# Performance work log

Measured on AMD Instinct MI355X. Metric: run time of the kernel, lower is better.

The kernel has to match this reference:

```python
import jax, jax.numpy as jnp
import numpy as np

POOL_SIZES = (1, 3, 6, 8)
EPS = 1e-5


def conv1x1(x, W, b):
    # x: [b, cin, h, w], W: [cout, cin], b: [cout]
    return jnp.einsum('bchw,oc->bohw', x, W) + b[None, :, None, None]


def ppm(x):
    # x: [b, c, h, w] -> [b, c, S] with S = sum(p*p); H,W divisible by each p
    b, c, h, w = x.shape
    outs = []
    for p in POOL_SIZES:
        pooled = x.reshape(b, c, p, h // p, p, w // p).mean(axis=(3, 5))
        outs.append(pooled.reshape(b, c, p * p))
    return jnp.concatenate(outs, axis=-1)


def setup_inputs() -> dict:
    key = jax.random.key(0)
    ks = jax.random.split(key, 8)
    B, Cin, H, W = 4, 512, 120, 120
    Ck, Cv, Cout = 256, 256, 512
    x = jax.random.normal(ks[0], (B, Cin, H, W), dtype=jnp.float32)
    sc = lambda cin: 1.0 / np.sqrt(cin)
    Wk = jax.random.normal(ks[1], (Ck, Cin), dtype=jnp.float32) * sc(Cin)
    bk = jnp.zeros((Ck,), jnp.float32)
    gamma = jnp.ones((Ck,), jnp.float32)
    beta = jnp.zeros((Ck,), jnp.float32)
    mean = jax.random.normal(ks[2], (Ck,), dtype=jnp.float32) * 0.1
    var = jax.random.uniform(ks[3], (Ck,), dtype=jnp.float32, minval=0.5, maxval=1.5)
    Wv = jax.random.normal(ks[4], (Cv, Cin), dtype=jnp.float32) * sc(Cin)
    bv = jnp.zeros((Cv,), jnp.float32)
    # original inits Conv_Out to zero; use random weights for a nontrivial baseline
    Wo = jax.random.normal(ks[5], (Cout, Cv), dtype=jnp.float32) * sc(Cv)
    bo = jnp.zeros((Cout,), jnp.float32)
    return {'x': x, 'Wk': Wk, 'bk': bk, 'gamma': gamma, 'beta': beta,
            'mean': mean, 'var': var, 'Wv': Wv, 'bv': bv, 'Wo': Wo, 'bo': bo}


def reference(x, Wk, bk, gamma, beta, mean, var, Wv, bv, Wo, bo):
    b, _, h, w = x.shape
    ck = Wk.shape[0]
    cv = Wv.shape[0]
    # shared Conv_Key / Conv_Query: conv1x1 -> BN (inference) -> ReLU
    kq = conv1x1(x, Wk, bk)
    inv = gamma / jnp.sqrt(var + EPS)
    kq = jax.nn.relu(kq * inv[None, :, None, None] + (beta - mean * inv)[None, :, None, None])
    value = ppm(conv1x1(x, Wv, bv)).transpose(0, 2, 1)      # [b, S, cv]
    key = ppm(kq)                                            # [b, ck, S]
    query = kq.reshape(b, ck, h * w).transpose(0, 2, 1)      # [b, hw, ck]
    scores = jnp.einsum('bnc,bcs->bns', query, key) * (ck ** -0.5)
    attn = jax.nn.softmax(scores, axis=-1)                   # [b, hw, S]
    agg = jnp.einsum('bns,bsv->bnv', attn, value)            # [b, hw, cv]
    agg = agg.transpose(0, 2, 1).reshape(b, cv, h, w)
    return conv1x1(agg, Wo, bo)
```

## Files before the change

kernel.cpp:

```cpp
#include <hip/hip_runtime.h>
#include <cstdint>
#include <cstddef>

#define HW 14400
#define WIDTH 120
#define S_TOT 110

typedef unsigned short u16;
typedef __attribute__((ext_vector_type(8))) short bf16x8;
typedef __attribute__((ext_vector_type(4))) float f32x4;

__device__ __forceinline__ u16 f2bf(float x) {
  unsigned u = __float_as_uint(x);
  unsigned r = (u + 0x7fffu + ((u >> 16) & 1u)) >> 16;
  return (u16)r;
}
__device__ __forceinline__ float bf2f(u16 h) {
  return __uint_as_float((unsigned)h << 16);
}

__device__ __forceinline__ void async16(void* lds, const void* g) {
  __builtin_amdgcn_global_load_lds(
      (const __attribute__((address_space(1))) void*)g,
      (__attribute__((address_space(3))) void*)lds, 16, 0, 0);
}

__global__ __launch_bounds__(256) void pool_kernel(const float* __restrict__ in,
                                                   float* __restrict__ outp) {
  __shared__ float part[576];
  const float* plane = in + (size_t)blockIdx.x * HW;
  int t = threadIdx.x;
  for (int bb = t; bb < 576; bb += 256) {
    int by = bb / 24, bx = bb % 24;
    const float* p0 = plane + (by * 5) * WIDTH + bx * 5;
    float s = 0.f;
#pragma unroll
    for (int yy = 0; yy < 5; ++yy)
#pragma unroll
      for (int xx = 0; xx < 5; ++xx) s += p0[yy * WIDTH + xx];
    part[bb] = s;
  }
  __syncthreads();
  if (t < S_TOT) {
    float s = 0.f;
    if (t == 0) {
      for (int i = 0; i < 576; ++i) s += part[i];
      s *= (1.f / 14400.f);
    } else if (t < 10) {
      int idx = t - 1, i = idx / 3, j = idx % 3;
      for (int a = 0; a < 8; ++a)
        for (int c = 0; c < 8; ++c) s += part[(i * 8 + a) * 24 + (j * 8 + c)];
      s *= (1.f / 1600.f);
    } else if (t < 46) {
      int idx = t - 10, i = idx / 6, j = idx % 6;
      for (int a = 0; a < 4; ++a)
        for (int c = 0; c < 4; ++c) s += part[(i * 4 + a) * 24 + (j * 4 + c)];
      s *= (1.f / 400.f);
    } else {
      int idx = t - 46, i = idx / 8, j = idx % 8;
      for (int a = 0; a < 3; ++a)
        for (int c = 0; c < 3; ++c) s += part[(i * 3 + a) * 24 + (j * 3 + c)];
      s *= (1.f / 225.f);
    }
    outp[(size_t)blockIdx.x * S_TOT + t] = s;
  }
}

__global__ __launch_bounds__(256) void convert_w(const float* __restrict__ in,
                                                 u16* __restrict__ hi,
                                                 u16* __restrict__ lo, int n) {
  int i = blockIdx.x * 256 + threadIdx.x;
  if (i < n) {
    float v = in[i];
    u16 h = f2bf(v);
    hi[i] = h;
    lo[i] = f2bf(v - bf2f(h));
  }
}

template <int CIN>
__global__ __launch_bounds__(256) void convert_t(const float* __restrict__ X,
                                                 u16* __restrict__ xth,
                                                 u16* __restrict__ xtl) {
  __shared__ float ls[64][65];
  int b = blockIdx.z;
  int n0 = blockIdx.x * 64, k0 = blockIdx.y * 64;
  int t = threadIdx.x;
  int rt = t >> 4, c4 = (t & 15) * 4;
#pragma unroll
  for (int rr = 0; rr < 4; ++rr) {
    int kk = rr * 16 + rt;
    float4 v = *(const float4*)&X[((size_t)(b * CIN + k0 + kk)) * HW + n0 + c4];
    ls[kk][c4] = v.x; ls[kk][c4 + 1] = v.y; ls[kk][c4 + 2] = v.z; ls[kk][c4 + 3] = v.w;
  }
  __syncthreads();
#pragma unroll
  for (int rr = 0; rr < 4; ++rr) {
    int nn = rr * 16 + rt;
    float v0 = ls[c4 + 0][nn], v1 = ls[c4 + 1][nn], v2 = ls[c4 + 2][nn], v3 = ls[c4 + 3][nn];
    ushort4 oh, ol;
    oh.x = f2bf(v0); ol.x = f2bf(v0 - bf2f(oh.x));
    oh.y = f2bf(v1); ol.y = f2bf(v1 - bf2f(oh.y));
    oh.z = f2bf(v2); ol.z = f2bf(v2 - bf2f(oh.z));
    oh.w = f2bf(v3); ol.w = f2bf(v3 - bf2f(oh.w));
    size_t idx = ((size_t)(b * HW + n0 + nn)) * CIN + k0 + c4;
    *(ushort4*)&xth[idx] = oh;
    *(ushort4*)&xtl[idx] = ol;
  }
}

template <int K, int M_TOT, bool BNRELU>
__global__ __launch_bounds__(256) void gemm_mfma(
    const u16* __restrict__ Ah, const u16* __restrict__ Al,
    const u16* __restrict__ Bh, const u16* __restrict__ Bl,
    float* __restrict__ C,
    const float* __restrict__ p0, const float* __restrict__ p1,
    const float* __restrict__ p2, const float* __restrict__ p3,
    const float* __restrict__ p4) {
  constexpr int NSTEP = K / 32;
  __shared__ alignas(16) u16 sAh[256 * 32];
  __shared__ alignas(16) u16 sAl[256 * 32];
  __shared__ alignas(16) u16 sBh[64 * 32];
  __shared__ alignas(16) u16 sBl[64 * 32];
  __shared__ float sP0[256], sP1[256];

  int t = threadIdx.x, w = t >> 6, l = t & 63;
  int b = blockIdx.z;
  int n0 = blockIdx.x * 64;
  int m0 = blockIdx.y * 256;

  if (BNRELU) {
    int m = m0 + t;
    float iv = p1[m] * rsqrtf(p4[m] + 1e-5f);
    sP0[t] = iv;
    sP1[t] = (p0[m] - p3[m]) * iv + p2[m];
  } else {
    sP0[t] = p0[m0 + t];
  }

  int crow = l >> 2;
  int cbyte = (l & 3) * 16;
  const size_t bOff = (size_t)b * HW;

  f32x4 acc[4][4];
#pragma unroll
  for (int i = 0; i < 4; ++i)
#pragma unroll
    for (int j = 0; j < 4; ++j) acc[i][j] = (f32x4){0.f, 0.f, 0.f, 0.f};

  int fr = l & 15, fk = (l >> 4) * 8;

  for (int ks = 0; ks < NSTEP; ++ks) {
    int k0 = ks * 32;
#pragma unroll
    for (int c = 0; c < 10; ++c) {
      int i = w * 10 + c;
      const u16* g;
      u16* d;
      if (i < 16) {
        g = Ah + (size_t)(m0 + i * 16 + crow) * K + k0;
        d = sAh + i * 512;
      } else if (i < 32) {
        g = Al + (size_t)(m0 + (i - 16) * 16 + crow) * K + k0;
        d = sAl + (i - 16) * 512;
      } else if (i < 36) {
        g = Bh + (bOff + n0 + (i - 32) * 16 + crow) * K + k0;
        d = sBh + (i - 32) * 512;
      } else {
        g = Bl + (bOff + n0 + (i - 36) * 16 + crow) * K + k0;
        d = sBl + (i - 36) * 512;
      }
      async16((char*)d, (const char*)g + cbyte);
    }
    __syncthreads();

    bf16x8 ah[4], al[4], bh[4], bl[4];
#pragma unroll
    for (int mt = 0; mt < 4; ++mt) {
      int r = w * 64 + mt * 16 + fr;
      ah[mt] = *(const bf16x8*)&sAh[r * 32 + fk];
      al[mt] = *(const bf16x8*)&sAl[r * 32 + fk];
    }
#pragma unroll
    for (int nt = 0; nt < 4; ++nt) {
      int r = nt * 16 + fr;
      bh[nt] = *(const bf16x8*)&sBh[r * 32 + fk];
      bl[nt] = *(const bf16x8*)&sBl[r * 32 + fk];
    }
#pragma unroll
    for (int mt = 0; mt < 4; ++mt)
#pragma unroll
      for (int nt = 0; nt < 4; ++nt) {
        acc[mt][nt] = __builtin_amdgcn_mfma_f32_16x16x32_bf16(ah[mt], bh[nt], acc[mt][nt], 0, 0, 0);
        acc[mt][nt] = __builtin_amdgcn_mfma_f32_16x16x32_bf16(ah[mt], bl[nt], acc[mt][nt], 0, 0, 0);
        acc[mt][nt] = __builtin_amdgcn_mfma_f32_16x16x32_bf16(al[mt], bh[nt], acc[mt][nt], 0, 0, 0);
      }
    __syncthreads();
  }

#pragma unroll
  for (int mt = 0; mt < 4; ++mt) {
    int lmBase = w * 64 + mt * 16 + (l >> 4) * 4;
#pragma unroll
    for (int nt = 0; nt < 4; ++nt) {
      int n = n0 + nt * 16 + fr;
#pragma unroll
      for (int r = 0; r < 4; ++r) {
        int lm = lmBase + r;
        float v = acc[mt][nt][r];
        if (BNRELU)
          v = fmaxf(v * sP0[lm] + sP1[lm], 0.f);
        else
          v = v + sP0[lm];
        C[((size_t)(b * M_TOT + m0 + lm)) * HW + n] = v;
      }
    }
  }
}

__global__ __launch_bounds__(256) void value_kernel(
    const float* __restrict__ Wv, const float* __restrict__ xp,
    const float* __restrict__ bv, u16* __restrict__ vth,
    u16* __restrict__ vtl) {
  int b = blockIdx.x >> 7, s = blockIdx.x & 127;
  int t = threadIdx.x;
  size_t o = ((size_t)(b * 256 + t)) * 128 + s;
  if (s >= S_TOT) { vth[o] = 0; vtl[o] = 0; return; }
  __shared__ float xs[512];
  for (int i = t; i < 512; i += 256) xs[i] = xp[((size_t)b * 512 + i) * S_TOT + s];
  __syncthreads();
  float accv = 0.f;
  const float* wv = Wv + (size_t)t * 512;
  for (int k = 0; k < 512; k += 4) {
    float4 w4 = *(const float4*)&wv[k];
    accv += w4.x * xs[k] + w4.y * xs[k + 1] + w4.z * xs[k + 2] + w4.w * xs[k + 3];
  }
  accv += bv[t];
  u16 h = f2bf(accv);
  vth[o] = h;
  vtl[o] = f2bf(accv - bf2f(h));
}

__global__ __launch_bounds__(256) void convert_key(const float* __restrict__ keyp,
                                                   u16* __restrict__ kth,
                                                   u16* __restrict__ ktl) {
  int b = blockIdx.x;
  int t = threadIdx.x;
  for (int i = t; i < 128 * 256; i += 256) {
    int s = i >> 8, c = i & 255;
    float v = (s < S_TOT) ? keyp[((size_t)(b * 256 + c)) * S_TOT + s] : 0.f;
    u16 h = f2bf(v);
    size_t o = ((size_t)(b * 128 + s)) * 256 + c;
    kth[o] = h;
    ktl[o] = f2bf(v - bf2f(h));
  }
}

__global__ __launch_bounds__(256) void attn_mfma(
    const u16* __restrict__ qh, const u16* __restrict__ ql,
    const u16* __restrict__ kh, const u16* __restrict__ kl,
    const u16* __restrict__ vh, const u16* __restrict__ vl,
    u16* __restrict__ aggh, u16* __restrict__ aggl) {
  __shared__ u16 Ph[64][136];
  __shared__ u16 Pl[64][136];
  int b = blockIdx.y, pix0 = blockIdx.x * 64;
  int t = threadIdx.x, w = t >> 6, l = t & 63;
  int fr = l & 15, q = l >> 4, fk = q * 8;

  f32x4 acc[7];
#pragma unroll
  for (int st = 0; st < 7; ++st) acc[st] = (f32x4){0.f, 0.f, 0.f, 0.f};

  const u16* qbh = qh + ((size_t)(b * HW + pix0 + w * 16 + fr)) * 256 + fk;
  const u16* qbl = ql + ((size_t)(b * HW + pix0 + w * 16 + fr)) * 256 + fk;
  const u16* kbh = kh + ((size_t)(b * 128 + fr)) * 256 + fk;
  const u16* kbl = kl + ((size_t)(b * 128 + fr)) * 256 + fk;

  for (int c0 = 0; c0 < 256; c0 += 32) {
    bf16x8 ah = *(const bf16x8*)(qbh + c0);
    bf16x8 al = *(const bf16x8*)(qbl + c0);
#pragma unroll
    for (int st = 0; st < 7; ++st) {
      bf16x8 bh = *(const bf16x8*)(kbh + (size_t)st * 16 * 256 + c0);
      bf16x8 bl = *(const bf16x8*)(kbl + (size_t)st * 16 * 256 + c0);
      acc[st] = __builtin_amdgcn_mfma_f32_16x16x32_bf16(ah, bh, acc[st], 0, 0, 0);
      acc[st] = __builtin_amdgcn_mfma_f32_16x16x32_bf16(ah, bl, acc[st], 0, 0, 0);
      acc[st] = __builtin_amdgcn_mfma_f32_16x16x32_bf16(al, bh, acc[st], 0, 0, 0);
    }
  }

#pragma unroll
  for (int st = 0; st < 7; ++st)
#pragma unroll
    for (int r = 0; r < 4; ++r) acc[st][r] *= 0.0625f;
  if (fr >= 14) {
#pragma unroll
    for (int r = 0; r < 4; ++r) acc[6][r] = -1e30f;
  }

#pragma unroll
  for (int r = 0; r < 4; ++r) {
    float m = -1e30f;
#pragma unroll
    for (int st = 0; st < 7; ++st) m = fmaxf(m, acc[st][r]);
    m = fmaxf(m, __shfl_xor(m, 1));
    m = fmaxf(m, __shfl_xor(m, 2));
    m = fmaxf(m, __shfl_xor(m, 4));
    m = fmaxf(m, __shfl_xor(m, 8));
    float s = 0.f;
#pragma unroll
    for (int st = 0; st < 7; ++st) {
      float e = __expf(acc[st][r] - m);
      acc[st][r] = e;
      s += e;
    }
    s += __shfl_xor(s, 1);
    s += __shfl_xor(s, 2);
    s += __shfl_xor(s, 4);
    s += __shfl_xor(s, 8);
    float inv = 1.f / s;
#pragma unroll
    for (int st = 0; st < 7; ++st) acc[st][r] *= inv;
  }

  int prow = w * 16 + q * 4;
#pragma unroll
  for (int st = 0; st < 7; ++st) {
    int s = st * 16 + fr;
#pragma unroll
    for (int r = 0; r < 4; ++r) {
      float v = acc[st][r];
      u16 h = f2bf(v);
      Ph[prow + r][s] = h;
      Pl[prow + r][s] = f2bf(v - bf2f(h));
    }
  }
  for (int i = t; i < 64 * 16; i += 256) {
    int rr = i >> 4, ss = 112 + (i & 15);
    Ph[rr][ss] = 0;
    Pl[rr][ss] = 0;
  }
  __syncthreads();

  f32x4 oacc[16];
#pragma unroll
  for (int nt = 0; nt < 16; ++nt) oacc[nt] = (f32x4){0.f, 0.f, 0.f, 0.f};

  const u16* vbh = vh + ((size_t)(b * 256 + fr)) * 128 + fk;
  const u16* vbl = vl + ((size_t)(b * 256 + fr)) * 128 + fk;

#pragma unroll
  for (int kc = 0; kc < 4; ++kc) {
    bf16x8 ah = *(const bf16x8*)&Ph[w * 16 + fr][kc * 32 + fk];
    bf16x8 al = *(const bf16x8*)&Pl[w * 16 + fr][kc * 32 + fk];
#pragma unroll
    for (int nt = 0; nt < 16; ++nt) {
      bf16x8 bh = *(const bf16x8*)(vbh + (size_t)nt * 16 * 128 + kc * 32);
      bf16x8 bl = *(const bf16x8*)(vbl + (size_t)nt * 16 * 128 + kc * 32);
      oacc[nt] = __builtin_amdgcn_mfma_f32_16x16x32_bf16(ah, bh, oacc[nt], 0, 0, 0);
      oacc[nt] = __builtin_amdgcn_mfma_f32_16x16x32_bf16(ah, bl, oacc[nt], 0, 0, 0);
      oacc[nt] = __builtin_amdgcn_mfma_f32_16x16x32_bf16(al, bh, oacc[nt], 0, 0, 0);
    }
  }

#pragma unroll
  for (int nt = 0; nt < 16; ++nt) {
    int cv = nt * 16 + fr;
#pragma unroll
    for (int r = 0; r < 4; ++r) {
      int pix = pix0 + w * 16 + q * 4 + r;
      float v = oacc[nt][r];
      u16 h = f2bf(v);
      size_t o = ((size_t)(b * HW + pix)) * 256 + cv;
      aggh[o] = h;
      aggl[o] = f2bf(v - bf2f(h));
    }
  }
}

extern "C" void kernel_launch(void* const* d_in, const int* in_sizes, int n_in,
                              void* d_out, int out_size, void* d_ws, size_t ws_size,
                              hipStream_t stream) {
  (void)in_sizes; (void)n_in; (void)out_size; (void)ws_size;
  const float* x     = (const float*)d_in[0];
  const float* Wk    = (const float*)d_in[1];
  const float* bk    = (const float*)d_in[2];
  const float* gamma = (const float*)d_in[3];
  const float* beta  = (const float*)d_in[4];
  const float* mean  = (const float*)d_in[5];
  const float* var   = (const float*)d_in[6];
  const float* Wv    = (const float*)d_in[7];
  const float* bv    = (const float*)d_in[8];
  const float* Wo    = (const float*)d_in[9];
  const float* bo    = (const float*)d_in[10];
  float* out = (float*)d_out;

  char* p = (char*)d_ws;
  float* kq = (float*)p;      p += (size_t)14745600 * 4;
  u16* xth = (u16*)p;         p += (size_t)29491200 * 2;
  u16* xtl = (u16*)p;         p += (size_t)29491200 * 2;
  u16* wkh = (u16*)p;         p += 131072 * 2;
  u16* wkl = (u16*)p;         p += 131072 * 2;
  u16* woh = (u16*)p;         p += 131072 * 2;
  u16* wol = (u16*)p;         p += 131072 * 2;
  float* xp = (float*)p;      p += (size_t)4 * 512 * 110 * 4;
  float* keyp = (float*)p;    p += (size_t)4 * 256 * 110 * 4;
  u16* vth = (u16*)p;         p += (size_t)4 * 256 * 128 * 2;
  u16* vtl = (u16*)p;         p += (size_t)4 * 256 * 128 * 2;
  u16* kth = (u16*)p;         p += (size_t)4 * 128 * 256 * 2;
  u16* ktl = (u16*)p;         p += (size_t)4 * 128 * 256 * 2;
  u16* aggh = xth;
  u16* kqth = xth + (size_t)14745600;
  u16* aggl = xtl;
  u16* kqtl = xtl + (size_t)14745600;

  convert_w<<<512, 256, 0, stream>>>(Wk, wkh, wkl, 256 * 512);
  convert_w<<<512, 256, 0, stream>>>(Wo, woh, wol, 512 * 256);
  convert_t<512><<<dim3(225, 8, 4), 256, 0, stream>>>(x, xth, xtl);
  pool_kernel<<<dim3(4 * 512), dim3(256), 0, stream>>>(x, xp);
  value_kernel<<<dim3(4 * 128), dim3(256), 0, stream>>>(Wv, xp, bv, vth, vtl);
  gemm_mfma<512, 256, true><<<dim3(225, 1, 4), 256, 0, stream>>>(
      wkh, wkl, xth, xtl, kq, bk, gamma, beta, mean, var);
  convert_t<256><<<dim3(225, 4, 4), 256, 0, stream>>>(kq, kqth, kqtl);
  pool_kernel<<<dim3(4 * 256), dim3(256), 0, stream>>>(kq, keyp);
  convert_key<<<dim3(4), dim3(256), 0, stream>>>(keyp, kth, ktl);
  attn_mfma<<<dim3(225, 4), 256, 0, stream>>>(kqth, kqtl, kth, ktl, vth, vtl,
                                              aggh, aggl);
  gemm_mfma<256, 512, false><<<dim3(225, 2, 4), 256, 0, stream>>>(
      woh, wol, aggh, aggl, out, bo, nullptr, nullptr, nullptr, nullptr);
}
```

Baseline: 619.5 us.

## Stage keys in LDS with async double buffering and retile PV GEMM

In the attention kernel, key tiles are now loaded into a double-buffered LDS region with async global-to-LDS copies, so the four waves share them instead of each reading them from global memory. The PV GEMM is re-partitioned so each wave owns 64 value channels across all 64 pixels, with P held in registers and V as the A operand. This lets the output be written as 4-element vector stores instead of scattered 2-byte stores. The score tile is padded to 8 sub-tiles, with the padding masked to -inf, which adds some extra MFMA work and extra barriers.

New measurement: 548.7 us. -11.4%, faster.

```diff
diff --git a/kernel.cpp b/kernel.cpp
--- a/kernel.cpp
+++ b/kernel.cpp
@@ -261,28 +261,46 @@
     const u16* __restrict__ kh, const u16* __restrict__ kl,
     const u16* __restrict__ vh, const u16* __restrict__ vl,
     u16* __restrict__ aggh, u16* __restrict__ aggl) {
-  __shared__ u16 Ph[64][136];
-  __shared__ u16 Pl[64][136];
+  __shared__ alignas(16) u16 lds[17408];
   int b = blockIdx.y, pix0 = blockIdx.x * 64;
   int t = threadIdx.x, w = t >> 6, l = t & 63;
-  int fr = l & 15, q = l >> 4, fk = q * 8;
-
-  f32x4 acc[7];
-#pragma unroll
-  for (int st = 0; st < 7; ++st) acc[st] = (f32x4){0.f, 0.f, 0.f, 0.f};
-
-  const u16* qbh = qh + ((size_t)(b * HW + pix0 + w * 16 + fr)) * 256 + fk;
-  const u16* qbl = ql + ((size_t)(b * HW + pix0 + w * 16 + fr)) * 256 + fk;
-  const u16* kbh = kh + ((size_t)(b * 128 + fr)) * 256 + fk;
-  const u16* kbl = kl + ((size_t)(b * 128 + fr)) * 256 + fk;
-
-  for (int c0 = 0; c0 < 256; c0 += 32) {
-    bf16x8 ah = *(const bf16x8*)(qbh + c0);
-    bf16x8 al = *(const bf16x8*)(qbl + c0);
-#pragma unroll
-    for (int st = 0; st < 7; ++st) {
-      bf16x8 bh = *(const bf16x8*)(kbh + (size_t)st * 16 * 256 + c0);
-      bf16x8 bl = *(const bf16x8*)(kbl + (size_t)st * 16 * 256 + c0);
+  int fr = l & 15, q = l >> 4;
+
+  const u16* kbase_h = kh + (size_t)b * 128 * 256;
+  const u16* kbase_l = kl + (size_t)b * 128 * 256;
+
+  f32x4 acc[8];
+#pragma unroll
+  for (int st = 0; st < 8; ++st) acc[st] = (f32x4){0.f, 0.f, 0.f, 0.f};
+
+  const u16* qbh = qh + ((size_t)(b * HW + pix0 + w * 16 + fr)) * 256 + q * 8;
+  const u16* qbl = ql + ((size_t)(b * HW + pix0 + w * 16 + fr)) * 256 + q * 8;
+
+  auto stageK = [&](int ks, int buf) {
+    int c0 = ks * 32;
+#pragma unroll
+    for (int j = 0; j < 4; ++j) {
+      int i = t + j * 256;
+      int half = i >> 9;
+      int idx = i & 511;
+      int st = idx >> 6, ll = idx & 63;
+      const u16* src = (half ? kbase_l : kbase_h) +
+                       (st * 16 + (ll & 15)) * 256 + c0 + (ll >> 4) * 8;
+      async16(&lds[buf * 8192 + half * 4096 + idx * 8], src);
+    }
+  };
+
+  stageK(0, 0);
+  for (int ks = 0; ks < 8; ++ks) {
+    __syncthreads();
+    if (ks < 7) stageK(ks + 1, (ks + 1) & 1);
+    bf16x8 ah = *(const bf16x8*)(qbh + ks * 32);
+    bf16x8 al = *(const bf16x8*)(qbl + ks * 32);
+    const u16* kb = &lds[(ks & 1) * 8192 + l * 8];
+#pragma unroll
+    for (int st = 0; st < 8; ++st) {
+      bf16x8 bh = *(const bf16x8*)(kb + st * 512);
+      bf16x8 bl = *(const bf16x8*)(kb + 4096 + st * 512);
       acc[st] = __builtin_amdgcn_mfma_f32_16x16x32_bf16(ah, bh, acc[st], 0, 0, 0);
       acc[st] = __builtin_amdgcn_mfma_f32_16x16x32_bf16(ah, bl, acc[st], 0, 0, 0);
       acc[st] = __builtin_amdgcn_mfma_f32_16x16x32_bf16(al, bh, acc[st], 0, 0, 0);
@@ -290,26 +308,28 @@
   }
 
 #pragma unroll
-  for (int st = 0; st < 7; ++st)
+  for (int st = 0; st < 8; ++st)
 #pragma unroll
     for (int r = 0; r < 4; ++r) acc[st][r] *= 0.0625f;
   if (fr >= 14) {
 #pragma unroll
     for (int r = 0; r < 4; ++r) acc[6][r] = -1e30f;
   }
+#pragma unroll
+  for (int r = 0; r < 4; ++r) acc[7][r] = -1e30f;
 
 #pragma unroll
   for (int r = 0; r < 4; ++r) {
     float m = -1e30f;
 #pragma unroll
-    for (int st = 0; st < 7; ++st) m = fmaxf(m, acc[st][r]);
+    for (int st = 0; st < 8; ++st) m = fmaxf(m, acc[st][r]);
     m = fmaxf(m, __shfl_xor(m, 1));
     m = fmaxf(m, __shfl_xor(m, 2));
     m = fmaxf(m, __shfl_xor(m, 4));
     m = fmaxf(m, __shfl_xor(m, 8));
     float s = 0.f;
 #pragma unroll
-    for (int st = 0; st < 7; ++st) {
+    for (int st = 0; st < 8; ++st) {
       float e = __expf(acc[st][r] - m);
       acc[st][r] = e;
       s += e;
@@ -320,60 +340,69 @@
     s += __shfl_xor(s, 8);
     float inv = 1.f / s;
 #pragma unroll
-    for (int st = 0; st < 7; ++st) acc[st][r] *= inv;
-  }
+    for (int st = 0; st < 8; ++st) acc[st][r] *= inv;
+  }
+
+  __syncthreads();
 
   int prow = w * 16 + q * 4;
 #pragma unroll
-  for (int st = 0; st < 7; ++st) {
+  for (int st = 0; st < 8; ++st) {
     int s = st * 16 + fr;
 #pragma unroll
     for (int r = 0; r < 4; ++r) {
       float v = acc[st][r];
       u16 h = f2bf(v);
-      Ph[prow + r][s] = h;
-      Pl[prow + r][s] = f2bf(v - bf2f(h));
-    }
-  }
-  for (int i = t; i < 64 * 16; i += 256) {
-    int rr = i >> 4, ss = 112 + (i & 15);
-    Ph[rr][ss] = 0;
-    Pl[rr][ss] = 0;
+      lds[(prow + r) * 136 + s] = h;
+      lds[8704 + (prow + r) * 136 + s] = f2bf(v - bf2f(h));
+    }
   }
   __syncthreads();
 
-  f32x4 oacc[16];
-#pragma unroll
-  for (int nt = 0; nt < 16; ++nt) oacc[nt] = (f32x4){0.f, 0.f, 0.f, 0.f};
-
-  const u16* vbh = vh + ((size_t)(b * 256 + fr)) * 128 + fk;
-  const u16* vbl = vl + ((size_t)(b * 256 + fr)) * 128 + fk;
+  f32x4 oacc[4][4];
+#pragma unroll
+  for (int nt = 0; nt < 4; ++nt)
+#pragma unroll
+    for (int pt = 0; pt < 4; ++pt) oacc[nt][pt] = (f32x4){0.f, 0.f, 0.f, 0.f};
+
+  const u16* vbh = vh + ((size_t)(b * 256 + w * 64 + fr)) * 128 + q * 8;
+  const u16* vbl = vl + ((size_t)(b * 256 + w * 64 + fr)) * 128 + q * 8;
 
 #pragma unroll
   for (int kc = 0; kc < 4; ++kc) {
-    bf16x8 ah = *(const bf16x8*)&Ph[w * 16 + fr][kc * 32 + fk];
-    bf16x8 al = *(const bf16x8*)&Pl[w * 16 + fr][kc * 32 + fk];
-#pragma unroll
-    for (int nt = 0; nt < 16; ++nt) {
-      bf16x8 bh = *(const bf16x8*)(vbh + (size_t)nt * 16 * 128 + kc * 32);
-      bf16x8 bl = *(const bf16x8*)(vbl + (size_t)nt * 16 * 128 + kc * 32);
-      oacc[nt] = __builtin_amdgcn_mfma_f32_16x16x32_bf16(ah, bh, oacc[nt], 0, 0, 0);
-      oacc[nt] = __builtin_amdgcn_mfma_f32_16x16x32_bf16(ah, bl, oacc[nt], 0, 0, 0);
-      oacc[nt] = __builtin_amdgcn_mfma_f32_16x16x32_bf16(al, bh, oacc[nt], 0, 0, 0);
-    }
-  }
-
-#pragma unroll
-  for (int nt = 0; nt < 16; ++nt) {
-    int cv = nt * 16 + fr;
-#pragma unroll
-    for (int r = 0; r < 4; ++r) {
-      int pix = pix0 + w * 16 + q * 4 + r;
-      float v = oacc[nt][r];
-      u16 h = f2bf(v);
-      size_t o = ((size_t)(b * HW + pix)) * 256 + cv;
-      aggh[o] = h;
-      aggl[o] = f2bf(v - bf2f(h));
+    bf16x8 ph[4], pl[4];
+#pragma unroll
+    for (int pt = 0; pt < 4; ++pt) {
+      ph[pt] = *(const bf16x8*)&lds[(pt * 16 + fr) * 136 + kc * 32 + q * 8];
+      pl[pt] = *(const bf16x8*)&lds[8704 + (pt * 16 + fr) * 136 + kc * 32 + q * 8];
+    }
+#pragma unroll
+    for (int nt = 0; nt < 4; ++nt) {
+      bf16x8 a_h = *(const bf16x8*)(vbh + (size_t)nt * 16 * 128 + kc * 32);
+      bf16x8 a_l = *(const bf16x8*)(vbl + (size_t)nt * 16 * 128 + kc * 32);
+#pragma unroll
+      for (int pt = 0; pt < 4; ++pt) {
+        oacc[nt][pt] = __builtin_amdgcn_mfma_f32_16x16x32_bf16(a_h, ph[pt], oacc[nt][pt], 0, 0, 0);
+        oacc[nt][pt] = __builtin_amdgcn_mfma_f32_16x16x32_bf16(a_h, pl[pt], oacc[nt][pt], 0, 0, 0);
+        oacc[nt][pt] = __builtin_amdgcn_mfma_f32_16x16x32_bf16(a_l, ph[pt], oacc[nt][pt], 0, 0, 0);
+      }
+    }
+  }
+
+#pragma unroll
+  for (int nt = 0; nt < 4; ++nt) {
+#pragma unroll
+    for (int pt = 0; pt < 4; ++pt) {
+      ushort4 oh, ol;
+      float v0 = oacc[nt][pt][0], v1 = oacc[nt][pt][1];
+      float v2 = oacc[nt][pt][2], v3 = oacc[nt][pt][3];
+      oh.x = f2bf(v0); ol.x = f2bf(v0 - bf2f(oh.x));
+      oh.y = f2bf(v1); ol.y = f2bf(v1 - bf2f(oh.y));
+      oh.z = f2bf(v2); ol.z = f2bf(v2 - bf2f(oh.z));
+      oh.w = f2bf(v3); ol.w = f2bf(v3 - bf2f(oh.w));
+      size_t o = ((size_t)(b * HW + pix0 + pt * 16 + fr)) * 256 + (w * 4 + nt) * 16 + q * 4;
+      *(ushort4*)&aggh[o] = oh;
+      *(ushort4*)&aggl[o] = ol;
     }
   }
 }
```
